# Kernel tuning notes

Hardware: AMD Instinct MI355X
Metric: run time of the kernel (lower is better)

Reference implementation:

```python
import jax, jax.numpy as jnp
import numpy as np

N_EPOCH = 1000
LR = 1e-3      # torch.optim.Adam defaults
BETA1 = 0.9
BETA2 = 0.999
EPS = 1e-8


def setup_inputs() -> dict:
    key = jax.random.key(0)
    k1, k2 = jax.random.split(key)
    H = jax.random.normal(k1, (128, 2048), dtype=jnp.float32)        # test activations [n_test, d]
    H_train = jax.random.normal(k2, (2048, 2048), dtype=jnp.float32)  # corpus activations [n_train, d]
    return {"H": H, "H_train": H_train}


def reference(H, H_train):
    n_test, n_train = H.shape[0], H_train.shape[0]

    def loss_fn(P):
        W = jax.nn.softmax(P, axis=-1)              # [n_test, n_train]
        H_approx = W @ H_train                       # einsum ij,jk->ik
        return jnp.sum((H_approx - H) ** 2)

    grad_fn = jax.grad(loss_fn)

    P0 = jnp.zeros((n_test, n_train), dtype=H.dtype)
    m0 = jnp.zeros_like(P0)
    v0 = jnp.zeros_like(P0)

    def adam_step(carry, t):
        P, m, v = carry
        g = grad_fn(P)
        m = BETA1 * m + (1.0 - BETA1) * g
        v = BETA2 * v + (1.0 - BETA2) * (g * g)
        m_hat = m / (1.0 - BETA1 ** t)
        v_hat = v / (1.0 - BETA2 ** t)
        P = P - LR * m_hat / (jnp.sqrt(v_hat) + EPS)
        return (P, m, v), None

    steps = jnp.arange(1, N_EPOCH + 1, dtype=H.dtype)  # 1-based Adam step count
    (P, _, _), _ = jax.lax.scan(adam_step, (P0, m0, v0), steps)
    return jax.nn.softmax(P, axis=-1)
```

## Files before the change

### kernel.cpp

```cpp
#include <hip/hip_runtime.h>
#include <math.h>

#define DN 2048
#define NT 128

#define KS   16
#define KSL  128
#define KCH  16
#define CB   128
#define RB   64

constexpr float LR    = 1e-3f;
constexpr float BETA1 = 0.9f;
constexpr float BETA2 = 0.999f;
constexpr float EPSA  = 1e-8f;

__device__ __forceinline__ float f4get(const float4& v, int k) {
    return k == 0 ? v.x : (k == 1 ? v.y : (k == 2 ? v.z : v.w));
}

__global__ __launch_bounds__(512, 4)
void wa_kernel(const float* __restrict__ W, const float* __restrict__ A,
               float* __restrict__ parts)
{
    __shared__ __align__(16) float At[2][KCH][CB];
    const int colb  = blockIdx.x * CB;
    const int rowb  = blockIdx.y * RB;
    const int kb    = blockIdx.z;
    const int kbase = kb * KSL;
    const int tx    = threadIdx.x;
    const int lane  = tx & 63;
    const int wid   = __builtin_amdgcn_readfirstlane(tx >> 6);
    const int row0  = rowb + wid * 8;

    const float* wbase = W + (size_t)row0 * DN + kbase;

    const int s_kr = tx >> 5;
    const int s_c4 = tx & 31;

    float2 acc[8];
    #pragma unroll
    for (int r = 0; r < 8; ++r) acc[r] = {0.f, 0.f};

    {
        const float* src = A + (size_t)(kbase + 0 * KCH) * DN + colb;
        *(float4*)&At[0][s_kr][s_c4 * 4] =
            *(const float4*)&src[(size_t)s_kr * DN + s_c4 * 4];
    }
    __syncthreads();

    #pragma unroll 1
    for (int ch = 0; ch < KSL / KCH; ++ch) {
        if (ch + 1 < KSL / KCH) {
            const float* src = A + (size_t)(kbase + (ch + 1) * KCH) * DN + colb;
            *(float4*)&At[(ch + 1) & 1][s_kr][s_c4 * 4] =
                *(const float4*)&src[(size_t)s_kr * DN + s_c4 * 4];
        }
        const int buf = ch & 1;
        #pragma unroll
        for (int kc = 0; kc < KCH / 4; ++kc) {
            float4 wv[8];
            #pragma unroll
            for (int r = 0; r < 8; ++r)
                wv[r] = *(const float4*)(wbase + (size_t)r * DN + ch * KCH + kc * 4);
            #pragma unroll
            for (int kk = 0; kk < 4; ++kk) {
                const float2 av = *(const float2*)&At[buf][4 * kc + kk][lane * 2];
                #pragma unroll
                for (int r = 0; r < 8; ++r) {
                    const float wk = f4get(wv[r], kk);
                    acc[r].x += wk * av.x;
                    acc[r].y += wk * av.y;
                }
            }
        }
        __syncthreads();
    }

    float* op = parts + (size_t)kb * (NT * DN) + colb + lane * 2;
    #pragma unroll
    for (int r = 0; r < 8; ++r)
        *(float2*)&op[(size_t)(row0 + r) * DN] = acc[r];
}

__global__ __launch_bounds__(512)
void bpart_kernel(const float* __restrict__ L, const float* __restrict__ R,
                  float* __restrict__ out_parts)
{
    __shared__ __align__(16) float Ws[128][36];
    __shared__ __align__(16) float At[32][36];
    const int j0    = blockIdx.x * 32;
    const int kbase = blockIdx.y * 512;
    const int tx = threadIdx.x;
    const int cg = tx & 7;
    const int rg = tx >> 3;
    float4 acc0 = {0.f, 0.f, 0.f, 0.f};
    float4 acc1 = {0.f, 0.f, 0.f, 0.f};

    for (int s = 0; s < 16; ++s) {
        const int k0 = kbase + s * 32;
        {
            int idx = tx;
            #pragma unroll
            for (int rr = 0; rr < 2; ++rr) {
                const int row = idx >> 3, f = idx & 7;
                const float4 wv = *(const float4*)&L[row * DN + k0 + 4 * f];
                *(float4*)&Ws[row][4 * f] = wv;
                idx += 512;
            }
            if (tx < 256) {
                const int c = tx >> 3, f = tx & 7;
                const float4 av = *(const float4*)&R[(size_t)(j0 + c) * DN + k0 + 4 * f];
                At[4 * f + 0][c] = av.x;
                At[4 * f + 1][c] = av.y;
                At[4 * f + 2][c] = av.z;
                At[4 * f + 3][c] = av.w;
            }
        }
        __syncthreads();
        #pragma unroll
        for (int kq = 0; kq < 8; ++kq) {
            const float4 w0 = *(const float4*)&Ws[rg][4 * kq];
            const float4 w1 = *(const float4*)&Ws[rg + 64][4 * kq];
            #pragma unroll
            for (int kk = 0; kk < 4; ++kk) {
                const float4 av = *(const float4*)&At[4 * kq + kk][4 * cg];
                const float wa = f4get(w0, kk);
                const float wb = f4get(w1, kk);
                acc0.x += wa * av.x; acc0.y += wa * av.y;
                acc0.z += wa * av.z; acc0.w += wa * av.w;
                acc1.x += wb * av.x; acc1.y += wb * av.y;
                acc1.z += wb * av.z; acc1.w += wb * av.w;
            }
        }
        __syncthreads();
    }
    float* op = out_parts + (size_t)blockIdx.y * (NT * DN);
    *(float4*)&op[rg * DN + j0 + 4 * cg] = acc0;
    *(float4*)&op[(rg + 64) * DN + j0 + 4 * cg] = acc1;
}

__global__ __launch_bounds__(256)
void gram_kernel(const float* __restrict__ Ht, float* __restrict__ A)
{
    __shared__ __align__(16) float Ti[64][36];
    __shared__ __align__(16) float Tj[64][36];
    const int i0 = blockIdx.x * 64, j0 = blockIdx.y * 64;
    const int tx = threadIdx.x;
    const int ti = tx & 15;
    const int tj = tx >> 4;
    float4 acc[4];
    #pragma unroll
    for (int a = 0; a < 4; ++a) acc[a] = {0.f, 0.f, 0.f, 0.f};

    for (int s = 0; s < 64; ++s) {
        const int k0 = s * 32;
        {
            int idx = tx;
            #pragma unroll
            for (int rr = 0; rr < 2; ++rr) {
                const int row = idx >> 3, f = idx & 7;
                *(float4*)&Ti[row][4 * f] = *(const float4*)&Ht[(size_t)(i0 + row) * DN + k0 + 4 * f];
                *(float4*)&Tj[row][4 * f] = *(const float4*)&Ht[(size_t)(j0 + row) * DN + k0 + 4 * f];
                idx += 256;
            }
        }
        __syncthreads();
        #pragma unroll
        for (int kq = 0; kq < 8; ++kq) {
            float4 iv[4], jv[4];
            #pragma unroll
            for (int a = 0; a < 4; ++a) iv[a] = *(const float4*)&Ti[ti + 16 * a][4 * kq];
            #pragma unroll
            for (int b = 0; b < 4; ++b) jv[b] = *(const float4*)&Tj[4 * tj + b][4 * kq];
            #pragma unroll
            for (int kk = 0; kk < 4; ++kk) {
                #pragma unroll
                for (int a = 0; a < 4; ++a) {
                    const float wa = f4get(iv[a], kk);
                    acc[a].x += wa * f4get(jv[0], kk);
                    acc[a].y += wa * f4get(jv[1], kk);
                    acc[a].z += wa * f4get(jv[2], kk);
                    acc[a].w += wa * f4get(jv[3], kk);
                }
            }
        }
        __syncthreads();
    }
    #pragma unroll
    for (int a = 0; a < 4; ++a)
        *(float4*)&A[(size_t)(i0 + ti + 16 * a) * DN + j0 + 4 * tj] = acc[a];
}

__global__ void sumB_kernel(const float* __restrict__ parts, float* __restrict__ Bm)
{
    const int idx = (blockIdx.x * 256 + threadIdx.x) * 4;
    float4 a = *(const float4*)&parts[idx];
    const float4 b = *(const float4*)&parts[(size_t)NT * DN + idx];
    const float4 c = *(const float4*)&parts[(size_t)2 * NT * DN + idx];
    const float4 d = *(const float4*)&parts[(size_t)3 * NT * DN + idx];
    a.x += b.x; a.x += c.x; a.x += d.x;
    a.y += b.y; a.y += c.y; a.y += d.y;
    a.z += b.z; a.z += c.z; a.z += d.z;
    a.w += b.w; a.w += c.w; a.w += d.w;
    *(float4*)&Bm[idx] = a;
}

__global__ void init_kernel(float* __restrict__ P, float* __restrict__ M,
                            float* __restrict__ V, float* __restrict__ W)
{
    const int idx = (blockIdx.x * 256 + threadIdx.x) * 4;
    const float4 z = {0.f, 0.f, 0.f, 0.f};
    const float u = 1.f / (float)DN;
    const float4 uu = {u, u, u, u};
    *(float4*)&P[idx] = z;
    *(float4*)&M[idx] = z;
    *(float4*)&V[idx] = z;
    *(float4*)&W[idx] = uu;
}

__device__ __forceinline__ float blk_sum(float x) {
    #pragma unroll
    for (int o = 32; o > 0; o >>= 1) x += __shfl_down(x, o);
    __shared__ float r[8];
    const int tx = threadIdx.x;
    if ((tx & 63) == 0) r[tx >> 6] = x;
    __syncthreads();
    x = ((r[0] + r[1]) + (r[2] + r[3])) + ((r[4] + r[5]) + (r[6] + r[7]));
    __syncthreads();
    return x;
}

__device__ __forceinline__ float blk_max(float x) {
    #pragma unroll
    for (int o = 32; o > 0; o >>= 1) x = fmaxf(x, __shfl_down(x, o));
    __shared__ float r[8];
    const int tx = threadIdx.x;
    if ((tx & 63) == 0) r[tx >> 6] = x;
    __syncthreads();
    x = fmaxf(fmaxf(fmaxf(r[0], r[1]), fmaxf(r[2], r[3])),
              fmaxf(fmaxf(r[4], r[5]), fmaxf(r[6], r[7])));
    __syncthreads();
    return x;
}

__global__ __launch_bounds__(512)
void adam_kernel(const float* __restrict__ parts, const float* __restrict__ Bm,
                 float* __restrict__ W, float* __restrict__ P,
                 float* __restrict__ M, float* __restrict__ V,
                 const float bc1, const float bc2)
{
    const int i = blockIdx.x;
    const int tx = threadIdx.x;
    const int base = i * DN + tx * 4;

    float4 s = {0.f, 0.f, 0.f, 0.f};
    #pragma unroll
    for (int p = 0; p < KS; ++p) {
        const float4 x = *(const float4*)&parts[(size_t)p * (NT * DN) + base];
        s.x += x.x; s.y += x.y; s.z += x.z; s.w += x.w;
    }
    const float4 b = *(const float4*)&Bm[base];
    float G4[4] = { 2.f * (s.x - b.x), 2.f * (s.y - b.y),
                    2.f * (s.z - b.z), 2.f * (s.w - b.w) };

    float W4[4], P4[4], M4[4], V4[4], E4[4];
    *(float4*)&W4[0] = *(const float4*)&W[base];

    float sp = 0.f;
    #pragma unroll
    for (int e = 0; e < 4; ++e) sp += W4[e] * G4[e];
    const float srow = blk_sum(sp);

    *(float4*)&P4[0] = *(const float4*)&P[base];
    *(float4*)&M4[0] = *(const float4*)&M[base];
    *(float4*)&V4[0] = *(const float4*)&V[base];

    float mx = -1e30f;
    #pragma unroll
    for (int e = 0; e < 4; ++e) {
        const float g  = W4[e] * (G4[e] - srow);
        const float m_ = BETA1 * M4[e] + (1.f - BETA1) * g;
        const float v_ = BETA2 * V4[e] + (1.f - BETA2) * g * g;
        M4[e] = m_; V4[e] = v_;
        const float mh = m_ * bc1;
        const float vh = v_ * bc2;
        const float pn = P4[e] - LR * mh / (sqrtf(vh) + EPSA);
        P4[e] = pn;
        mx = fmaxf(mx, pn);
    }
    mx = blk_max(mx);

    float es = 0.f;
    #pragma unroll
    for (int e = 0; e < 4; ++e) { E4[e] = expf(P4[e] - mx); es += E4[e]; }
    const float sig = blk_sum(es);
    #pragma unroll
    for (int e = 0; e < 4; ++e) W4[e] = E4[e] / sig;

    *(float4*)&W[base] = *(const float4*)&W4[0];
    *(float4*)&P[base] = *(const float4*)&P4[0];
    *(float4*)&M[base] = *(const float4*)&M4[0];
    *(float4*)&V[base] = *(const float4*)&V4[0];
}

extern "C" void kernel_launch(void* const* d_in, const int* in_sizes, int n_in,
                              void* d_out, int out_size, void* d_ws, size_t ws_size,
                              hipStream_t stream)
{
    const float* H  = (const float*)d_in[0];
    const float* Ht = (const float*)d_in[1];

    float* ws = (float*)d_ws;
    float* A     = ws;
    float* Bm    = A  + (size_t)DN * DN;
    float* P     = Bm + (size_t)NT * DN;
    float* M     = P  + (size_t)NT * DN;
    float* V     = M  + (size_t)NT * DN;
    float* W     = V  + (size_t)NT * DN;
    float* parts = W  + (size_t)NT * DN;

    gram_kernel<<<dim3(32, 32), 256, 0, stream>>>(Ht, A);
    bpart_kernel<<<dim3(64, 4), 512, 0, stream>>>(H, Ht, parts);
    sumB_kernel<<<256, 256, 0, stream>>>(parts, Bm);
    init_kernel<<<256, 256, 0, stream>>>(P, M, V, W);

    double b1t = 1.0, b2t = 1.0;
    for (int t = 1; t <= 1000; ++t) {
        b1t *= 0.9; b2t *= 0.999;
        wa_kernel<<<dim3(DN / CB, NT / RB, KS), 512, 0, stream>>>(W, A, parts);
        const float bc1 = (float)(1.0 / (1.0 - b1t));
        const float bc2 = (float)(1.0 / (1.0 - b2t));
        adam_kernel<<<NT, 512, 0, stream>>>(parts, Bm, W, P, M, V, bc1, bc2);
    }

    hipMemcpyAsync(d_out, W, (size_t)NT * DN * sizeof(float),
                   hipMemcpyDeviceToDevice, stream);
}
```

Baseline: 30.21 ms.

## Retile wa_kernel into 4x4 register tiles with W staged in shared memory

Restructures the W@A partial-product kernel. The block tile changes from 64x128 to 32x256, and the whole 32x128 W slice is staged in LDS up front instead of each wave streaming W rows from global memory. Each thread now computes a 4x4 output tile from LDS float4 loads, which raises FMA-per-load reuse compared with the earlier 8x2 tile that used scalar-broadcast W. The cost is extra LDS use for the padded W tile, which may lower occupancy, plus a different grid shape.

```diff
diff --git a/kernel.cpp b/kernel.cpp
--- a/kernel.cpp
+++ b/kernel.cpp
@@ -7,8 +7,8 @@
 #define KS   16
 #define KSL  128
 #define KCH  16
-#define CB   128
-#define RB   64
+#define CB   256
+#define RB   32
 
 constexpr float LR    = 1e-3f;
 constexpr float BETA1 = 0.9f;
@@ -23,71 +23,92 @@
 void wa_kernel(const float* __restrict__ W, const float* __restrict__ A,
                float* __restrict__ parts)
 {
-    __shared__ __align__(16) float At[2][KCH][CB];
+    __shared__ __align__(16) float Ws[32][132];
+    __shared__ __align__(16) float As[2][KCH][CB];
     const int colb  = blockIdx.x * CB;
     const int rowb  = blockIdx.y * RB;
     const int kb    = blockIdx.z;
     const int kbase = kb * KSL;
     const int tx    = threadIdx.x;
     const int lane  = tx & 63;
-    const int wid   = __builtin_amdgcn_readfirstlane(tx >> 6);
-    const int row0  = rowb + wid * 8;
-
-    const float* wbase = W + (size_t)row0 * DN + kbase;
-
-    const int s_kr = tx >> 5;
-    const int s_c4 = tx & 31;
-
-    float2 acc[8];
-    #pragma unroll
-    for (int r = 0; r < 8; ++r) acc[r] = {0.f, 0.f};
-
-    {
-        const float* src = A + (size_t)(kbase + 0 * KCH) * DN + colb;
-        *(float4*)&At[0][s_kr][s_c4 * 4] =
-            *(const float4*)&src[(size_t)s_kr * DN + s_c4 * 4];
-    }
-    __syncthreads();
+    const int wv    = tx >> 6;
+    const int wr    = wv >> 2;
+    const int wc    = wv & 3;
+    const int rl    = lane >> 4;
+    const int lc    = lane & 15;
+    const int rloc  = wr * 16 + rl * 4;
+    const int cloc  = wc * 64 + lc * 4;
+
+    #pragma unroll
+    for (int it = 0; it < 2; ++it) {
+        const int f = it * 512 + tx;
+        const int r = f >> 5, k4 = f & 31;
+        *(float4*)&Ws[r][k4 * 4] =
+            *(const float4*)&W[(size_t)(rowb + r) * DN + kbase + k4 * 4];
+    }
+    #pragma unroll
+    for (int it = 0; it < 2; ++it) {
+        const int f = it * 512 + tx;
+        const int kr = f >> 6, c4 = f & 63;
+        *(float4*)&As[0][kr][c4 * 4] =
+            *(const float4*)&A[(size_t)(kbase + kr) * DN + colb + c4 * 4];
+    }
+    __syncthreads();
+
+    float4 acc[4];
+    #pragma unroll
+    for (int i = 0; i < 4; ++i) acc[i] = {0.f, 0.f, 0.f, 0.f};
+
+    const int s_kr = tx >> 6 << 1;
 
     #pragma unroll 1
     for (int ch = 0; ch < KSL / KCH; ++ch) {
         if (ch + 1 < KSL / KCH) {
-            const float* src = A + (size_t)(kbase + (ch + 1) * KCH) * DN + colb;
-            *(float4*)&At[(ch + 1) & 1][s_kr][s_c4 * 4] =
-                *(const float4*)&src[(size_t)s_kr * DN + s_c4 * 4];
+            #pragma unroll
+            for (int it = 0; it < 2; ++it) {
+                const int f = it * 512 + tx;
+                const int kr = f >> 6, c4 = f & 63;
+                *(float4*)&As[(ch + 1) & 1][kr][c4 * 4] =
+                    *(const float4*)&A[(size_t)(kbase + (ch + 1) * KCH + kr) * DN + colb + c4 * 4];
+            }
         }
         const int buf = ch & 1;
         #pragma unroll
-        for (int kc = 0; kc < KCH / 4; ++kc) {
-            float4 wv[8];
-            #pragma unroll
-            for (int r = 0; r < 8; ++r)
-                wv[r] = *(const float4*)(wbase + (size_t)r * DN + ch * KCH + kc * 4);
+        for (int kq = 0; kq < KCH / 4; ++kq) {
+            const int kk0 = ch * KCH + kq * 4;
+            float4 wf[4], af[4];
+            #pragma unroll
+            for (int i = 0; i < 4; ++i)
+                wf[i] = *(const float4*)&Ws[rloc + i][kk0];
+            #pragma unroll
+            for (int kk = 0; kk < 4; ++kk)
+                af[kk] = *(const float4*)&As[buf][kq * 4 + kk][cloc];
             #pragma unroll
             for (int kk = 0; kk < 4; ++kk) {
-                const float2 av = *(const float2*)&At[buf][4 * kc + kk][lane * 2];
                 #pragma unroll
-                for (int r = 0; r < 8; ++r) {
-                    const float wk = f4get(wv[r], kk);
-                    acc[r].x += wk * av.x;
-                    acc[r].y += wk * av.y;
+                for (int i = 0; i < 4; ++i) {
+                    const float wk = f4get(wf[i], kk);
+                    acc[i].x += wk * af[kk].x;
+                    acc[i].y += wk * af[kk].y;
+                    acc[i].z += wk * af[kk].z;
+                    acc[i].w += wk * af[kk].w;
                 }
             }
         }
         __syncthreads();
     }
 
-    float* op = parts + (size_t)kb * (NT * DN) + colb + lane * 2;
-    #pragma unroll
-    for (int r = 0; r < 8; ++r)
-        *(float2*)&op[(size_t)(row0 + r) * DN] = acc[r];
+    float* op = parts + (size_t)kb * (NT * DN) + colb + cloc;
+    #pragma unroll
+    for (int i = 0; i < 4; ++i)
+        *(float4*)&op[(size_t)(rowb + rloc + i) * DN] = acc[i];
 }
 
 __global__ __launch_bounds__(512)
 void bpart_kernel(const float* __restrict__ L, const float* __restrict__ R,
                   float* __restrict__ out_parts)
 {
-    __shared__ __align__(16) float Ws[128][36];
+    __shared__ __align__(16) float Wsh[128][36];
     __shared__ __align__(16) float At[32][36];
     const int j0    = blockIdx.x * 32;
     const int kbase = blockIdx.y * 512;
@@ -105,7 +126,7 @@
             for (int rr = 0; rr < 2; ++rr) {
                 const int row = idx >> 3, f = idx & 7;
                 const float4 wv = *(const float4*)&L[row * DN + k0 + 4 * f];
-                *(float4*)&Ws[row][4 * f] = wv;
+                *(float4*)&Wsh[row][4 * f] = wv;
                 idx += 512;
             }
             if (tx < 256) {
@@ -120,8 +141,8 @@
         __syncthreads();
         #pragma unroll
         for (int kq = 0; kq < 8; ++kq) {
-            const float4 w0 = *(const float4*)&Ws[rg][4 * kq];
-            const float4 w1 = *(const float4*)&Ws[rg + 64][4 * kq];
+            const float4 w0 = *(const float4*)&Wsh[rg][4 * kq];
+            const float4 w1 = *(const float4*)&Wsh[rg + 64][4 * kq];
             #pragma unroll
             for (int kk = 0; kk < 4; ++kk) {
                 const float4 av = *(const float4*)&At[4 * kq + kk][4 * cg];
```

Result: faster. 28.80 ms (-4.7%).
